# Performance work log

Measured on AMD Instinct MI355X. Metric: run time of the kernel, lower is better.

Reference implementation:

```python
import jax, jax.numpy as jnp
import numpy as np

N_NODES = 50000
N_EDGES = 800000
DIM = 128
NEG_SLOPE = 0.2


def gat_conv(x, ei, W, a_src, a_dst, b):
    """PyG GATConv, heads=1, add_self_loops=True."""
    N = x.shape[0]
    h = x @ W  # [N, out]
    loop = jnp.arange(N, dtype=ei.dtype)
    src = jnp.concatenate([ei[0], loop])
    dst = jnp.concatenate([ei[1], loop])
    al = h @ a_src  # [N]
    ar = h @ a_dst  # [N]
    e = jax.nn.leaky_relu(al[src] + ar[dst], NEG_SLOPE)  # [E+N]
    m = jax.ops.segment_max(e, dst, num_segments=N)
    ex = jnp.exp(e - m[dst])
    s = jax.ops.segment_sum(ex, dst, num_segments=N)
    alpha = ex / s[dst]
    out = jax.ops.segment_sum(h[src] * alpha[:, None], dst, num_segments=N)
    return out + b


def setup_inputs() -> dict:
    key = jax.random.key(0)
    ks = jax.random.split(key, 32)
    sc = 1.0 / np.sqrt(DIM)
    inp = {"x": jax.random.normal(ks[0], (N_NODES, DIM), jnp.float32)}
    for i in range(5):
        inp[f"W{i+1}"] = jax.random.normal(ks[1 + 4 * i], (DIM, DIM), jnp.float32) * sc
        inp[f"as{i+1}"] = jax.random.normal(ks[2 + 4 * i], (DIM,), jnp.float32) * sc
        inp[f"ad{i+1}"] = jax.random.normal(ks[3 + 4 * i], (DIM,), jnp.float32) * sc
        inp[f"b{i+1}"] = jnp.zeros((DIM,), jnp.float32)
    inp["edge_index"] = jax.random.randint(ks[22], (2, N_EDGES), 0, N_NODES, jnp.int32)
    inp["edge_index_cross"] = jax.random.randint(ks[23], (2, N_EDGES), 0, N_NODES, jnp.int32)
    return inp


def reference(x, W1, as1, ad1, b1, W2, as2, ad2, b2, W3, as3, ad3, b3,
              W4, as4, ad4, b4, W5, as5, ad5, b5, edge_index, edge_index_cross):
    # dropout is identity in inference mode
    x = jax.nn.relu(gat_conv(x, edge_index, W1, as1, ad1, b1))
    x = jax.nn.relu(gat_conv(x, edge_index_cross, W2, as2, ad2, b2))
    x = jax.nn.relu(gat_conv(x, edge_index, W3, as3, ad3, b3))
    x = jax.nn.relu(gat_conv(x, edge_index_cross, W4, as4, ad4, b4))
    x = gat_conv(x, edge_index, W5, as5, ad5, b5)
    return jnp.squeeze(x)
```

## Files before the change

### kernel.cpp

```cpp
#include <hip/hip_runtime.h>

#define DIM 128
#define NEG 0.2f
#define CAP 128
#define BSZ 512
#define CB  256

typedef __attribute__((ext_vector_type(8))) short bf16x8;
typedef __attribute__((ext_vector_type(4))) float f32x4;
typedef __attribute__((ext_vector_type(8))) _Float16 h16x8;
typedef __attribute__((ext_vector_type(8))) unsigned short us8;

__device__ __forceinline__ float lrelu(float v) { return v > 0.f ? v : NEG * v; }

__device__ __forceinline__ unsigned short f2bf(float f) {
    unsigned u = __float_as_uint(f);
    unsigned r = (u + 0x7FFFu + ((u >> 16) & 1u)) >> 16;
    return (unsigned short)r;
}
__device__ __forceinline__ float bf2f(unsigned short h) {
    return __uint_as_float(((unsigned)h) << 16);
}


__global__ __launch_bounds__(256) void convert_x(const float* __restrict__ x,
                                                 unsigned short* __restrict__ hi,
                                                 unsigned short* __restrict__ lo, int n4) {
    int i = blockIdx.x * 256 + threadIdx.x;
    if (i >= n4) return;
    const int p = i * 4;
    const int tile = p >> 11, kc = (p >> 9) & 3, q = (p >> 7) & 3;
    const int rr = (p >> 3) & 15, j0 = p & 7;
    const int row = tile * 16 + rr;
    const int k = kc * 32 + q * 8 + j0;
    float4 v = *(const float4*)(x + (size_t)row * DIM + k);
    ushort4 h, l;
    h.x = f2bf(v.x); l.x = f2bf(v.x - bf2f(h.x));
    h.y = f2bf(v.y); l.y = f2bf(v.y - bf2f(h.y));
    h.z = f2bf(v.z); l.z = f2bf(v.z - bf2f(h.z));
    h.w = f2bf(v.w); l.w = f2bf(v.w - bf2f(h.w));
    *(ushort4*)(hi + p) = h;
    *(ushort4*)(lo + p) = l;
}

__global__ __launch_bounds__(256) void convert_w(const float* __restrict__ W0,
                                                 const float* __restrict__ W1,
                                                 const float* __restrict__ W2,
                                                 const float* __restrict__ W3,
                                                 const float* __restrict__ W4,
                                                 unsigned short* __restrict__ Bhi,
                                                 unsigned short* __restrict__ Blo) {
    const int Lyr = blockIdx.x >> 6;
    const float* W = (Lyr == 0) ? W0 : (Lyr == 1) ? W1 : (Lyr == 2) ? W2
                    : (Lyr == 3) ? W3 : W4;
    int i = (blockIdx.x & 63) * 256 + threadIdx.x;
    const int tt = i >> 11, kc = (i >> 9) & 3, q = (i >> 7) & 3;
    const int n = (i >> 3) & 15, j = i & 7;
    const int c = tt * 16 + n;
    const int k = kc * 32 + q * 8 + j;
    float v = W[k * 128 + c];
    unsigned short h = f2bf(v);
    Bhi[Lyr * 16384 + i] = h;
    Blo[Lyr * 16384 + i] = f2bf(v - bf2f(h));
}

__global__ __launch_bounds__(256) void gemm_mfma(const unsigned short* __restrict__ Ahi,
                                                 const unsigned short* __restrict__ Alo,
                                                 const unsigned short* __restrict__ Bhi,
                                                 const unsigned short* __restrict__ Blo,
                                                 const float* __restrict__ asrc,
                                                 const float* __restrict__ adst,
                                                 _Float16* __restrict__ Hh,
                                                 float* __restrict__ al,
                                                 float* __restrict__ ar, int N) {
    __shared__ unsigned short sBhi[16384];
    __shared__ unsigned short sBlo[16384];
    const int t = threadIdx.x;
    const int wv = t >> 6;
    const int l = t & 63;
    const int tile = blockIdx.x * 4 + wv;
    const int r0 = tile * 16;
    const int m = l & 15;
    const int q = l >> 4;

    bf16x8 ahi[4], alo[4];
    const size_t abase = (size_t)tile * 2048 + (size_t)l * 8;
#pragma unroll
    for (int kc = 0; kc < 4; ++kc) {
        ahi[kc] = *(const bf16x8*)(Ahi + abase + kc * 512);
        alo[kc] = *(const bf16x8*)(Alo + abase + kc * 512);
    }
    {
        const int4* gh = (const int4*)Bhi;
        const int4* gl = (const int4*)Blo;
        int4* sh = (int4*)sBhi;
        int4* sl = (int4*)sBlo;
#pragma unroll
        for (int r = 0; r < 8; ++r) {
            sh[t + 256 * r] = gh[t + 256 * r];
            sl[t + 256 * r] = gl[t + 256 * r];
        }
    }
    __syncthreads();

    f32x4 acc[8];
#pragma unroll
    for (int tt = 0; tt < 8; ++tt) acc[tt] = (f32x4){0.f, 0.f, 0.f, 0.f};

#pragma unroll
    for (int tt = 0; tt < 8; ++tt) {
#pragma unroll
        for (int kc = 0; kc < 4; ++kc) {
            const int boff = tt * 2048 + kc * 512 + l * 8;
            const bf16x8 bhi = *(const bf16x8*)(sBhi + boff);
            const bf16x8 blo = *(const bf16x8*)(sBlo + boff);
            acc[tt] = __builtin_amdgcn_mfma_f32_16x16x32_bf16(ahi[kc], bhi, acc[tt], 0, 0, 0);
            acc[tt] = __builtin_amdgcn_mfma_f32_16x16x32_bf16(ahi[kc], blo, acc[tt], 0, 0, 0);
            acc[tt] = __builtin_amdgcn_mfma_f32_16x16x32_bf16(alo[kc], bhi, acc[tt], 0, 0, 0);
        }
    }

#pragma unroll
    for (int j = 0; j < 4; ++j) {
        const int rr = r0 + q * 4 + j;
        if (rr < N) {
            _Float16* hp = Hh + (size_t)rr * DIM + m;
#pragma unroll
            for (int tt = 0; tt < 8; ++tt) hp[tt * 16] = (_Float16)acc[tt][j];
        }
    }

    float pa[4] = {0.f, 0.f, 0.f, 0.f};
    float pr[4] = {0.f, 0.f, 0.f, 0.f};
#pragma unroll
    for (int tt = 0; tt < 8; ++tt) {
        const float as = asrc[tt * 16 + m];
        const float ad = adst[tt * 16 + m];
#pragma unroll
        for (int j = 0; j < 4; ++j) {
            pa[j] += acc[tt][j] * as;
            pr[j] += acc[tt][j] * ad;
        }
    }
#pragma unroll
    for (int off = 8; off; off >>= 1) {
#pragma unroll
        for (int j = 0; j < 4; ++j) {
            pa[j] += __shfl_xor(pa[j], off);
            pr[j] += __shfl_xor(pr[j], off);
        }
    }
    if (m == 0) {
#pragma unroll
        for (int j = 0; j < 4; ++j) {
            const int rr = r0 + q * 4 + j;
            if (rr < N) { al[rr] = pa[j]; ar[rr] = pr[j]; }
        }
    }
}

__device__ __forceinline__ void edge_decode(int e, const int* ei, const int* eix,
                                            int E1, int N, int E2, int& src, int& d) {
    if (e < E1) {
        src = ei[e];
        d = ei[E1 + e];
    } else {
        int k = e - E1;
        src = eix[k];
        d = N + eix[E2 + k];
    }
}

__global__ __launch_bounds__(256) void csr_hist(const int* __restrict__ ei,
                                                const int* __restrict__ eix,
                                                int* __restrict__ g_hist,
                                                int E1, int E2, int N, int NB, int CE) {
    __shared__ int h[256];
    const int t = threadIdx.x;
    const int c = blockIdx.x;
    h[t] = 0;
    __syncthreads();
    const int Etot = E1 + E2;
    const int beg = c * CE;
    const int end = min(Etot, beg + CE);
    for (int e = beg + t; e < end; e += 256) {
        int src, d;
        edge_decode(e, ei, eix, E1, N, E2, src, d);
        atomicAdd(&h[d >> 9], 1);
    }
    __syncthreads();
    if (t < NB) g_hist[t * CB + c] = h[t];
}

__global__ __launch_bounds__(1024) void bsum_kernel(const int* __restrict__ in,
                                                    int* __restrict__ bsum, int L) {
    __shared__ int wsum[16];
    int t = threadIdx.x, wave = t >> 6, lane = t & 63;
    int i = blockIdx.x * 1024 + t;
    int v = (i < L) ? in[i] : 0;
#pragma unroll
    for (int off = 32; off; off >>= 1) v += __shfl_xor(v, off);
    if (lane == 0) wsum[wave] = v;
    __syncthreads();
    if (t == 0) {
        int s = 0;
#pragma unroll
        for (int j = 0; j < 16; ++j) s += wsum[j];
        bsum[blockIdx.x] = s;
    }
}

__global__ __launch_bounds__(128) void scan_small(int* __restrict__ bsum, int nb) {
    __shared__ int w0tot;
    int t = threadIdx.x;
    int v = (t < nb) ? bsum[t] : 0;
    int s = v;
#pragma unroll
    for (int off = 1; off < 64; off <<= 1) {
        int u = __shfl_up(s, off);
        if ((t & 63) >= off) s += u;
    }
    if (t == 63) w0tot = s;
    __syncthreads();
    if (t >= 64) s += w0tot;
    if (t < nb) bsum[t] = s - v;
}

__global__ __launch_bounds__(1024) void bscan_kernel(const int* __restrict__ in,
                                                     const int* __restrict__ bsum,
                                                     int* __restrict__ out, int L) {
    __shared__ int wsum[16];
    __shared__ int woff[16];
    int t = threadIdx.x, wave = t >> 6, lane = t & 63;
    int i = blockIdx.x * 1024 + t;
    int v = (i < L) ? in[i] : 0;
    int s = v;
#pragma unroll
    for (int off = 1; off < 64; off <<= 1) {
        int u = __shfl_up(s, off);
        if (lane >= off) s += u;
    }
    if (lane == 63) wsum[wave] = s;
    __syncthreads();
    if (t == 0) {
        int r = 0;
#pragma unroll
        for (int j = 0; j < 16; ++j) { woff[j] = r; r += wsum[j]; }
    }
    __syncthreads();
    if (i < L) out[i] = bsum[blockIdx.x] + woff[wave] + s - v;
}

__global__ __launch_bounds__(256) void csr_partition(const int* __restrict__ ei,
                                                     const int* __restrict__ eix,
                                                     const int* __restrict__ g_base,
                                                     unsigned* __restrict__ staging,
                                                     int E1, int E2, int N, int NB, int CE) {
    __shared__ int cur[256];
    const int t = threadIdx.x;
    const int c = blockIdx.x;
    if (t < NB) cur[t] = g_base[t * CB + c];
    __syncthreads();
    const int Etot = E1 + E2;
    const int beg = c * CE;
    const int end = min(Etot, beg + CE);
    for (int e = beg + t; e < end; e += 256) {
        int src, d;
        edge_decode(e, ei, eix, E1, N, E2, src, d);
        int p = atomicAdd(&cur[d >> 9], 1);
        staging[p] = ((unsigned)(d & (BSZ - 1)) << 22) | (unsigned)src;
    }
}

__global__ __launch_bounds__(256) void csr_finalize(const unsigned* __restrict__ staging,
                                                    const int* __restrict__ g_base,
                                                    int* __restrict__ row_off,
                                                    int* __restrict__ col,
                                                    int Ntot, int Etot, int NB) {
    __shared__ int cnt_s[BSZ];
    __shared__ int cur_s[BSZ];
    __shared__ int wsum[4], woff[4];
    const int t = threadIdx.x;
    const int k = blockIdx.x;
    cnt_s[t] = 0;
    cnt_s[t + 256] = 0;
    __syncthreads();
    const int seg_beg = g_base[k * CB];
    const int seg_end = (k == NB - 1) ? Etot : g_base[(k + 1) * CB];
    for (int i = seg_beg + t; i < seg_end; i += 256)
        atomicAdd(&cnt_s[staging[i] >> 22], 1);
    __syncthreads();

    const int a = cnt_s[2 * t], b = cnt_s[2 * t + 1];
    const int tsum = a + b;
    int s = tsum;
    const int lane = t & 63, wv = t >> 6;
#pragma unroll
    for (int off = 1; off < 64; off <<= 1) {
        int u = __shfl_up(s, off);
        if (lane >= off) s += u;
    }
    if (lane == 63) wsum[wv] = s;
    __syncthreads();
    if (t == 0) {
        int r = 0;
#pragma unroll
        for (int j = 0; j < 4; ++j) { woff[j] = r; r += wsum[j]; }
    }
    __syncthreads();
    const int excl = woff[wv] + s - tsum;
    cur_s[2 * t] = seg_beg + excl;
    cur_s[2 * t + 1] = seg_beg + excl + a;
    const int nbase = k * BSZ;
    if (nbase + 2 * t < Ntot)     row_off[nbase + 2 * t]     = seg_beg + excl;
    if (nbase + 2 * t + 1 < Ntot) row_off[nbase + 2 * t + 1] = seg_beg + excl + a;
    __syncthreads();
    for (int i = seg_beg + t; i < seg_end; i += 256) {
        unsigned v = staging[i];
        int p = atomicAdd(&cur_s[v >> 22], 1);
        col[p] = (int)(v & 0x3FFFFFu);
    }
    if (k == 0 && t == 0) row_off[Ntot] = Etot;
}

__global__ __launch_bounds__(256) void sort_nodes(const int* __restrict__ row_off,
                                                  int* __restrict__ perm, int N) {
    __shared__ int kdeg[256];
    __shared__ int kidx[256];
    const int t = threadIdx.x;
    const int w = blockIdx.x * 256 + t;
    kdeg[t] = (w < N) ? (row_off[w + 1] - row_off[w]) : -1;
    kidx[t] = w;
    __syncthreads();
#pragma unroll
    for (int ksz = 2; ksz <= 256; ksz <<= 1) {
        for (int jj = ksz >> 1; jj > 0; jj >>= 1) {
            const int ixj = t ^ jj;
            if (ixj > t) {
                const int d0 = kdeg[t], d1 = kdeg[ixj];
                const bool up = ((t & ksz) == 0);
                if ((d0 > d1) == up) {
                    kdeg[t] = d1; kdeg[ixj] = d0;
                    const int i0 = kidx[t]; kidx[t] = kidx[ixj]; kidx[ixj] = i0;
                }
            }
            __syncthreads();
        }
    }
    perm[blockIdx.x * 256 + t] = kidx[t];
}

__global__ __launch_bounds__(256) void agg_kernel(const _Float16* __restrict__ Hh,
                                                  const float* __restrict__ al,
                                                  const float* __restrict__ ar,
                                                  const int* __restrict__ row_off,
                                                  const int* __restrict__ col,
                                                  const int* __restrict__ perm,
                                                  const float* __restrict__ bias,
                                                  float* __restrict__ outF,
                                                  unsigned short* __restrict__ outHi,
                                                  unsigned short* __restrict__ outLo,
                                                  int N, int last) {
    __shared__ float salpha[16][CAP];
    __shared__ int   scol[16][CAP];
    const int t = threadIdx.x;
    const int wv = t >> 6;
    const int lane = t & 63;
    const int g = lane >> 4;
    const int j = lane & 15;
    const int slot = wv * 4 + g;
    const int w = perm[blockIdx.x * 16 + slot];
    if (w >= N) return;

    const int beg = row_off[w];
    const int deg = row_off[w + 1] - beg;
    const float arn = ar[w];
    const float vself = lrelu(al[w] + arn);

    float mm = -1e30f, ss = 0.f;
    for (int i = j; i < deg; i += 16) {
        const int c = col[beg + i];
        float v = lrelu(al[c] + arn);
        if (i < CAP) { scol[slot][i] = c; salpha[slot][i] = v; }
        float nm = fmaxf(mm, v);
        ss = ss * __expf(mm - nm) + __expf(v - nm);
        mm = nm;
    }
#pragma unroll
    for (int off = 8; off; off >>= 1) {
        float mo = __shfl_xor(mm, off);
        float so = __shfl_xor(ss, off);
        float nm = fmaxf(mm, mo);
        ss = ss * __expf(mm - nm) + so * __expf(mo - nm);
        mm = nm;
    }
    {
        float nm = fmaxf(mm, vself);
        ss = ss * __expf(mm - nm) + __expf(vself - nm);
        mm = nm;
    }
    const float m = mm;
    const float invs = 1.f / ss;

    const int capdeg = deg < CAP ? deg : CAP;
    for (int i = j; i < capdeg; i += 16)
        salpha[slot][i] = __expf(salpha[slot][i] - m) * invs;

    const float aself = __expf(vself - m) * invs;
    const h16x8 hs = *(const h16x8*)(Hh + (size_t)w * DIM + 8 * j);
    float acc[8];
#pragma unroll
    for (int k = 0; k < 8; ++k) acc[k] = aself * (float)hs[k];

    int i = 0;
    for (; i + 3 < deg; i += 4) {
        int sn0, sn1, sn2, sn3;
        float a0, a1, a2, a3;
        if (i + 3 < CAP) {
            sn0 = scol[slot][i];     a0 = salpha[slot][i];
            sn1 = scol[slot][i + 1]; a1 = salpha[slot][i + 1];
            sn2 = scol[slot][i + 2]; a2 = salpha[slot][i + 2];
            sn3 = scol[slot][i + 3]; a3 = salpha[slot][i + 3];
        } else {
            const int e = beg + i;
            sn0 = col[e]; sn1 = col[e + 1]; sn2 = col[e + 2]; sn3 = col[e + 3];
            a0 = __expf(lrelu(al[sn0] + arn) - m) * invs;
            a1 = __expf(lrelu(al[sn1] + arn) - m) * invs;
            a2 = __expf(lrelu(al[sn2] + arn) - m) * invs;
            a3 = __expf(lrelu(al[sn3] + arn) - m) * invs;
        }
        const h16x8 h0 = *(const h16x8*)(Hh + (size_t)sn0 * DIM + 8 * j);
        const h16x8 h1 = *(const h16x8*)(Hh + (size_t)sn1 * DIM + 8 * j);
        const h16x8 h2 = *(const h16x8*)(Hh + (size_t)sn2 * DIM + 8 * j);
        const h16x8 h3 = *(const h16x8*)(Hh + (size_t)sn3 * DIM + 8 * j);
#pragma unroll
        for (int k = 0; k < 8; ++k)
            acc[k] += a0 * (float)h0[k] + a1 * (float)h1[k] +
                      a2 * (float)h2[k] + a3 * (float)h3[k];
    }
    for (; i < deg; ++i) {
        int sn;
        float a;
        if (i < CAP) {
            sn = scol[slot][i];
            a = salpha[slot][i];
        } else {
            sn = col[beg + i];
            a = __expf(lrelu(al[sn] + arn) - m) * invs;
        }
        const h16x8 hv = *(const h16x8*)(Hh + (size_t)sn * DIM + 8 * j);
#pragma unroll
        for (int k = 0; k < 8; ++k) acc[k] += a * (float)hv[k];
    }

    const float4 b0 = *(const float4*)(bias + 8 * j);
    const float4 b1 = *(const float4*)(bias + 8 * j + 4);
    float o[8];
    o[0] = acc[0] + b0.x; o[1] = acc[1] + b0.y;
    o[2] = acc[2] + b0.z; o[3] = acc[3] + b0.w;
    o[4] = acc[4] + b1.x; o[5] = acc[5] + b1.y;
    o[6] = acc[6] + b1.z; o[7] = acc[7] + b1.w;
    if (last) {
        float4 o0 = make_float4(o[0], o[1], o[2], o[3]);
        float4 o1 = make_float4(o[4], o[5], o[6], o[7]);
        *(float4*)(outF + (size_t)w * DIM + 8 * j) = o0;
        *(float4*)(outF + (size_t)w * DIM + 8 * j + 4) = o1;
    } else {
        us8 hv, lv;
#pragma unroll
        for (int k = 0; k < 8; ++k) {
            float v = fmaxf(o[k], 0.f);
            unsigned short hb = f2bf(v);
            hv[k] = hb;
            lv[k] = f2bf(v - bf2f(hb));
        }
        const size_t p = (size_t)(w >> 4) * 2048 +
                         (size_t)((j >> 2) * 512 + (j & 3) * 128 + (w & 15) * 8);
        *(us8*)(outHi + p) = hv;
        *(us8*)(outLo + p) = lv;
    }
}

extern "C" void kernel_launch(void* const* d_in, const int* in_sizes, int n_in,
                              void* d_out, int out_size, void* d_ws, size_t ws_size,
                              hipStream_t stream) {
    const float* x = (const float*)d_in[0];
    const float* W[5];
    const float* asv[5];
    const float* adv[5];
    const float* bv[5];
    for (int i = 0; i < 5; ++i) {
        W[i]   = (const float*)d_in[1 + 4 * i];
        asv[i] = (const float*)d_in[2 + 4 * i];
        adv[i] = (const float*)d_in[3 + 4 * i];
        bv[i]  = (const float*)d_in[4 + 4 * i];
    }
    const int* ei  = (const int*)d_in[21];
    const int* eix = (const int*)d_in[22];
    const int N  = in_sizes[0] / DIM;
    const int E1 = in_sizes[21] / 2;
    const int E2 = in_sizes[22] / 2;
    const int Ntot = 2 * N;
    const int Etot = E1 + E2;
    const int NB = (Ntot + BSZ - 1) / BSZ;
    const int CE = (Etot + CB - 1) / CB;
    const int gemm_blocks = (N + 63) / 64;
    const size_t tiles_alloc = (size_t)gemm_blocks * 4;
    const int PW = (N + 255) / 256;
    const int PN = PW * 256;

    size_t off = 0;
    auto alloc = [&](size_t bytes) {
        void* r = (char*)d_ws + off;
        off += (bytes + 255) & ~(size_t)255;
        return r;
    };
    float* Hbuf  = (float*)alloc((size_t)N * DIM * sizeof(float));
    unsigned short* Xhi = (unsigned short*)alloc(tiles_alloc * 2048 * 2);
    unsigned short* Xlo = (unsigned short*)alloc(tiles_alloc * 2048 * 2);
    float* al    = (float*)alloc((size_t)N * sizeof(float));
    float* ar    = (float*)alloc((size_t)N * sizeof(float));
    unsigned short* wthi = (unsigned short*)alloc(5 * 16384 * 2);
    unsigned short* wtlo = (unsigned short*)alloc(5 * 16384 * 2);
    int* g_hist  = (int*)alloc((size_t)NB * CB * sizeof(int));
    int* g_base  = (int*)alloc((size_t)NB * CB * sizeof(int));
    int* bsum    = (int*)alloc(128 * sizeof(int));
    int* row     = (int*)alloc((size_t)(Ntot + 1) * sizeof(int));
    int* col     = (int*)alloc((size_t)Etot * sizeof(int));
    int* perm    = (int*)alloc((size_t)2 * PN * sizeof(int));
    (void)ws_size;
    unsigned* staging = (unsigned*)Hbuf;
    _Float16* Hh = (_Float16*)Hbuf;

    float* F = (float*)d_out;

    const int n4 = N * DIM / 4;
    convert_x<<<(n4 + 255) / 256, 256, 0, stream>>>(x, Xhi, Xlo, n4);
    convert_w<<<320, 256, 0, stream>>>(W[0], W[1], W[2], W[3], W[4], wthi, wtlo);

    const int L = NB * CB;
    const int nbb = (L + 1023) / 1024;
    csr_hist<<<CB, 256, 0, stream>>>(ei, eix, g_hist, E1, E2, N, NB, CE);
    bsum_kernel<<<nbb, 1024, 0, stream>>>(g_hist, bsum, L);
    scan_small<<<1, 128, 0, stream>>>(bsum, nbb);
    bscan_kernel<<<nbb, 1024, 0, stream>>>(g_hist, bsum, g_base, L);
    csr_partition<<<CB, 256, 0, stream>>>(ei, eix, g_base, staging, E1, E2, N, NB, CE);
    csr_finalize<<<NB, 256, 0, stream>>>(staging, g_base, row, col, Ntot, Etot, NB);

    sort_nodes<<<PW, 256, 0, stream>>>(row, perm, N);
    sort_nodes<<<PW, 256, 0, stream>>>(row + N, perm + PN, N);

    const int node_blocks = PN / 16;

    for (int Lyr = 0; Lyr < 5; ++Lyr) {
        gemm_mfma<<<gemm_blocks, 256, 0, stream>>>(Xhi, Xlo,
                                                   wthi + Lyr * 16384, wtlo + Lyr * 16384,
                                                   asv[Lyr], adv[Lyr], Hh, al, ar, N);
        const int half = (Lyr % 2 == 0) ? 0 : 1;
        const int* ro = row + half * N;
        const int* pm = perm + half * PN;
        agg_kernel<<<node_blocks, 256, 0, stream>>>(Hh, al, ar, ro, col, pm, bv[Lyr],
                                                    F, Xhi, Xlo, N, (Lyr == 4) ? 1 : 0);
    }
}
```

Measured before the change: 496.9 us.

## Drop max-subtraction softmax, remove degree sort, defer normalization to output

Attention weights are now computed as plain exp without the online running max, and the sum is reduced by a simple shuffle add. The 1/sum normalization moves to a single multiply at output time, so the second pass that rewrote the stored alphas is gone. The per-block degree-sorting kernels and the permutation indirection are removed, so nodes are processed in natural order. Shared arrays are padded to reduce bank conflicts. Without the max subtraction, exp can overflow if attention logits grow large, and losing the degree sort may leave more load imbalance across lanes.

```diff
diff --git a/kernel.cpp b/kernel.cpp
--- a/kernel.cpp
+++ b/kernel.cpp
@@ -3,6 +3,7 @@
 #define DIM 128
 #define NEG 0.2f
 #define CAP 128
+#define CPAD 129
 #define BSZ 512
 #define CB  256
 
@@ -323,94 +324,58 @@
     if (k == 0 && t == 0) row_off[Ntot] = Etot;
 }
 
-__global__ __launch_bounds__(256) void sort_nodes(const int* __restrict__ row_off,
-                                                  int* __restrict__ perm, int N) {
-    __shared__ int kdeg[256];
-    __shared__ int kidx[256];
-    const int t = threadIdx.x;
-    const int w = blockIdx.x * 256 + t;
-    kdeg[t] = (w < N) ? (row_off[w + 1] - row_off[w]) : -1;
-    kidx[t] = w;
-    __syncthreads();
-#pragma unroll
-    for (int ksz = 2; ksz <= 256; ksz <<= 1) {
-        for (int jj = ksz >> 1; jj > 0; jj >>= 1) {
-            const int ixj = t ^ jj;
-            if (ixj > t) {
-                const int d0 = kdeg[t], d1 = kdeg[ixj];
-                const bool up = ((t & ksz) == 0);
-                if ((d0 > d1) == up) {
-                    kdeg[t] = d1; kdeg[ixj] = d0;
-                    const int i0 = kidx[t]; kidx[t] = kidx[ixj]; kidx[ixj] = i0;
-                }
-            }
-            __syncthreads();
-        }
-    }
-    perm[blockIdx.x * 256 + t] = kidx[t];
-}
-
 __global__ __launch_bounds__(256) void agg_kernel(const _Float16* __restrict__ Hh,
                                                   const float* __restrict__ al,
                                                   const float* __restrict__ ar,
                                                   const int* __restrict__ row_off,
                                                   const int* __restrict__ col,
-                                                  const int* __restrict__ perm,
                                                   const float* __restrict__ bias,
                                                   float* __restrict__ outF,
                                                   unsigned short* __restrict__ outHi,
                                                   unsigned short* __restrict__ outLo,
                                                   int N, int last) {
-    __shared__ float salpha[16][CAP];
-    __shared__ int   scol[16][CAP];
+    __shared__ float salpha[16][CPAD];
+    __shared__ int   scol[16][CPAD];
     const int t = threadIdx.x;
     const int wv = t >> 6;
     const int lane = t & 63;
     const int g = lane >> 4;
     const int j = lane & 15;
     const int slot = wv * 4 + g;
-    const int w = perm[blockIdx.x * 16 + slot];
+    const int w = blockIdx.x * 16 + slot;
     if (w >= N) return;
 
     const int beg = row_off[w];
     const int deg = row_off[w + 1] - beg;
     const float arn = ar[w];
-    const float vself = lrelu(al[w] + arn);
-
-    float mm = -1e30f, ss = 0.f;
-    for (int i = j; i < deg; i += 16) {
-        const int c = col[beg + i];
-        float v = lrelu(al[c] + arn);
-        if (i < CAP) { scol[slot][i] = c; salpha[slot][i] = v; }
-        float nm = fmaxf(mm, v);
-        ss = ss * __expf(mm - nm) + __expf(v - nm);
-        mm = nm;
-    }
-#pragma unroll
-    for (int off = 8; off; off >>= 1) {
-        float mo = __shfl_xor(mm, off);
-        float so = __shfl_xor(ss, off);
-        float nm = fmaxf(mm, mo);
-        ss = ss * __expf(mm - nm) + so * __expf(mo - nm);
-        mm = nm;
-    }
-    {
-        float nm = fmaxf(mm, vself);
-        ss = ss * __expf(mm - nm) + __expf(vself - nm);
-        mm = nm;
-    }
-    const float m = mm;
+    const float eself = __expf(lrelu(al[w] + arn));
+
+    float ss = 0.f;
+    if (deg <= CAP) {
+        for (int i = j; i < deg; i += 16) {
+            const int c = col[beg + i];
+            float e = __expf(lrelu(al[c] + arn));
+            scol[slot][i] = c;
+            salpha[slot][i] = e;
+            ss += e;
+        }
+    } else {
+        for (int i = j; i < deg; i += 16) {
+            const int c = col[beg + i];
+            float e = __expf(lrelu(al[c] + arn));
+            if (i < CAP) { scol[slot][i] = c; salpha[slot][i] = e; }
+            ss += e;
+        }
+    }
+#pragma unroll
+    for (int off = 8; off; off >>= 1) ss += __shfl_xor(ss, off);
+    ss += eself;
     const float invs = 1.f / ss;
 
-    const int capdeg = deg < CAP ? deg : CAP;
-    for (int i = j; i < capdeg; i += 16)
-        salpha[slot][i] = __expf(salpha[slot][i] - m) * invs;
-
-    const float aself = __expf(vself - m) * invs;
     const h16x8 hs = *(const h16x8*)(Hh + (size_t)w * DIM + 8 * j);
     float acc[8];
 #pragma unroll
-    for (int k = 0; k < 8; ++k) acc[k] = aself * (float)hs[k];
+    for (int k = 0; k < 8; ++k) acc[k] = eself * (float)hs[k];
 
     int i = 0;
     for (; i + 3 < deg; i += 4) {
@@ -424,10 +389,10 @@
         } else {
             const int e = beg + i;
             sn0 = col[e]; sn1 = col[e + 1]; sn2 = col[e + 2]; sn3 = col[e + 3];
-            a0 = __expf(lrelu(al[sn0] + arn) - m) * invs;
-            a1 = __expf(lrelu(al[sn1] + arn) - m) * invs;
-            a2 = __expf(lrelu(al[sn2] + arn) - m) * invs;
-            a3 = __expf(lrelu(al[sn3] + arn) - m) * invs;
+            a0 = __expf(lrelu(al[sn0] + arn));
+            a1 = __expf(lrelu(al[sn1] + arn));
+            a2 = __expf(lrelu(al[sn2] + arn));
+            a3 = __expf(lrelu(al[sn3] + arn));
         }
         const h16x8 h0 = *(const h16x8*)(Hh + (size_t)sn0 * DIM + 8 * j);
         const h16x8 h1 = *(const h16x8*)(Hh + (size_t)sn1 * DIM + 8 * j);
@@ -446,7 +411,7 @@
             a = salpha[slot][i];
         } else {
             sn = col[beg + i];
-            a = __expf(lrelu(al[sn] + arn) - m) * invs;
+            a = __expf(lrelu(al[sn] + arn));
         }
         const h16x8 hv = *(const h16x8*)(Hh + (size_t)sn * DIM + 8 * j);
 #pragma unroll
@@ -456,10 +421,10 @@
     const float4 b0 = *(const float4*)(bias + 8 * j);
     const float4 b1 = *(const float4*)(bias + 8 * j + 4);
     float o[8];
-    o[0] = acc[0] + b0.x; o[1] = acc[1] + b0.y;
-    o[2] = acc[2] + b0.z; o[3] = acc[3] + b0.w;
-    o[4] = acc[4] + b1.x; o[5] = acc[5] + b1.y;
-    o[6] = acc[6] + b1.z; o[7] = acc[7] + b1.w;
+    o[0] = acc[0] * invs + b0.x; o[1] = acc[1] * invs + b0.y;
+    o[2] = acc[2] * invs + b0.z; o[3] = acc[3] * invs + b0.w;
+    o[4] = acc[4] * invs + b1.x; o[5] = acc[5] * invs + b1.y;
+    o[6] = acc[6] * invs + b1.z; o[7] = acc[7] * invs + b1.w;
     if (last) {
         float4 o0 = make_float4(o[0], o[1], o[2], o[3]);
         float4 o1 = make_float4(o[4], o[5], o[6], o[7]);
@@ -506,8 +471,6 @@
     const int CE = (Etot + CB - 1) / CB;
     const int gemm_blocks = (N + 63) / 64;
     const size_t tiles_alloc = (size_t)gemm_blocks * 4;
-    const int PW = (N + 255) / 256;
-    const int PN = PW * 256;
 
     size_t off = 0;
     auto alloc = [&](size_t bytes) {
@@ -527,7 +490,6 @@
     int* bsum    = (int*)alloc(128 * sizeof(int));
     int* row     = (int*)alloc((size_t)(Ntot + 1) * sizeof(int));
     int* col     = (int*)alloc((size_t)Etot * sizeof(int));
-    int* perm    = (int*)alloc((size_t)2 * PN * sizeof(int));
     (void)ws_size;
     unsigned* staging = (unsigned*)Hbuf;
     _Float16* Hh = (_Float16*)Hbuf;
@@ -547,19 +509,14 @@
     csr_partition<<<CB, 256, 0, stream>>>(ei, eix, g_base, staging, E1, E2, N, NB, CE);
     csr_finalize<<<NB, 256, 0, stream>>>(staging, g_base, row, col, Ntot, Etot, NB);
 
-    sort_nodes<<<PW, 256, 0, stream>>>(row, perm, N);
-    sort_nodes<<<PW, 256, 0, stream>>>(row + N, perm + PN, N);
-
-    const int node_blocks = PN / 16;
+    const int node_blocks = (N + 15) / 16;
 
     for (int Lyr = 0; Lyr < 5; ++Lyr) {
         gemm_mfma<<<gemm_blocks, 256, 0, stream>>>(Xhi, Xlo,
                                                    wthi + Lyr * 16384, wtlo + Lyr * 16384,
                                                    asv[Lyr], adv[Lyr], Hh, al, ar, N);
-        const int half = (Lyr % 2 == 0) ? 0 : 1;
-        const int* ro = row + half * N;
-        const int* pm = perm + half * PN;
-        agg_kernel<<<node_blocks, 256, 0, stream>>>(Hh, al, ar, ro, col, pm, bv[Lyr],
+        const int* ro = row + ((Lyr % 2 == 0) ? 0 : N);
+        agg_kernel<<<node_blocks, 256, 0, stream>>>(Hh, al, ar, ro, col, bv[Lyr],
                                                     F, Xhi, Xlo, N, (Lyr == 4) ? 1 : 0);
     }
 }
```

Result: faster. 408.2 us (-17.9%).
